# Kernel tuning notes

Hardware: AMD Instinct MI355X
Metric: run time of the kernel (lower is better)

## Reference

```python
import jax, jax.numpy as jnp
import numpy as np

N_HEADS = 16
LN_EPS = 1e-5


def _rope(x, sin, cos):
    # Faithful to source: uses x.shape[0] (batch here) as 'length'.
    L = x.shape[0]
    x1, x2 = x[..., ::2], x[..., 1::2]
    c = cos[:L, None, :]  # broadcasts over dim 1 (seq)
    s = sin[:L, None, :]
    return jnp.concatenate([x1 * c - x2 * s, x1 * s + x2 * c], axis=-1)


def _layer_norm(x):
    m = jnp.mean(x, axis=-1, keepdims=True)
    v = jnp.var(x, axis=-1, keepdims=True)
    return (x - m) * jax.lax.rsqrt(v + LN_EPS)


def setup_inputs() -> dict:
    key = jax.random.key(0)
    ks = jax.random.split(key, 8)
    B, S, D = 2, 2048, 2048
    CTX = 2048
    x = jax.random.normal(ks[0], (B, S, D), dtype=jnp.float32)
    scale = 0.02
    Wq = jax.random.normal(ks[1], (D, D), dtype=jnp.float32) * scale
    Wk = jax.random.normal(ks[2], (D, D), dtype=jnp.float32) * scale
    Wv = jax.random.normal(ks[3], (D, D), dtype=jnp.float32) * scale
    W1 = jax.random.normal(ks[4], (D, 4 * D), dtype=jnp.float32) * scale
    b1 = jnp.zeros((4 * D,), dtype=jnp.float32)
    W2 = jax.random.normal(ks[5], (4 * D, D), dtype=jnp.float32) * scale
    b2 = jnp.zeros((D,), dtype=jnp.float32)
    inv_freq = 1.0 / (10000.0 ** (jnp.arange(0, D, 2, dtype=jnp.float32) / D))
    sinusoid = jnp.einsum('i,j->ij', jnp.arange(CTX, dtype=jnp.float32), inv_freq)
    sin = jnp.sin(sinusoid)
    cos = jnp.cos(sinusoid)
    return {"x": x, "Wq": Wq, "Wk": Wk, "Wv": Wv, "W1": W1, "b1": b1,
            "W2": W2, "b2": b2, "sin": sin, "cos": cos, "i": 0}


def reference(x, Wq, Wk, Wv, W1, b1, W2, b2, sin, cos, i):
    B, S, D = x.shape
    H = N_HEADS
    hd = D // H
    q = _rope(x @ Wq, sin, cos)
    k = _rope(x @ Wk, sin, cos)
    v = x @ Wv
    # [B,S,D] -> [B,H,S,hd]
    q = q.reshape(B, S, H, hd).transpose(0, 2, 1, 3)
    k = k.reshape(B, S, H, hd).transpose(0, 2, 1, 3)
    v = v.reshape(B, S, H, hd).transpose(0, 2, 1, 3)
    attn = jnp.einsum('bhqd,bhkd->bhqk', q, k) / jnp.sqrt(jnp.float32(hd))
    causal = jnp.tril(jnp.ones((S, S), dtype=bool))
    attn = jnp.where(causal[None, None], attn, -jnp.inf)
    attn = jax.nn.softmax(attn, axis=-1)
    out = jnp.einsum('bhqk,bhkd->bhqd', attn, v)
    out = out.transpose(0, 2, 1, 3).reshape(B, S, D)
    out = _layer_norm(out + x)
    h = jax.nn.gelu(out @ W1 + b1, approximate=False)
    out2 = _layer_norm(h @ W2 + b2 + out)
    return out2
```

## Files before the change

### kernel.cpp

```cpp
#include <hip/hip_runtime.h>
#include <hip/hip_bf16.h>
#include <math.h>
#include <stdint.h>

using bf16 = __hip_bfloat16;
typedef __attribute__((ext_vector_type(4))) float f32x4;
typedef __attribute__((ext_vector_type(8))) short s16x8;

#define MFMA16(a, b, c) __builtin_amdgcn_mfma_f32_16x16x32_bf16(a, b, c, 0, 0, 0)

__device__ __forceinline__ void gload_lds16(const void* g, void* l) {
    __builtin_amdgcn_global_load_lds(
        (const __attribute__((address_space(1))) void*)g,
        (__attribute__((address_space(3))) void*)l, 16, 0, 0);
}

struct alignas(16) bf16x8s { bf16 v[8]; };

__global__ void cvt_f32_bf16(const float* __restrict__ in, bf16* __restrict__ out, long n) {
    long i = ((long)blockIdx.x * 256 + threadIdx.x) * 8;
    if (i >= n) return;
    float4 a = *(const float4*)(in + i);
    float4 b = *(const float4*)(in + i + 4);
    bf16x8s r;
    r.v[0] = __float2bfloat16(a.x); r.v[1] = __float2bfloat16(a.y);
    r.v[2] = __float2bfloat16(a.z); r.v[3] = __float2bfloat16(a.w);
    r.v[4] = __float2bfloat16(b.x); r.v[5] = __float2bfloat16(b.y);
    r.v[6] = __float2bfloat16(b.z); r.v[7] = __float2bfloat16(b.w);
    *(bf16x8s*)(out + i) = r;
}

__global__ void transpose_cvt(const float* __restrict__ W, bf16* __restrict__ Wt, int K, int N) {
    __shared__ bf16 t[32][33];
    int tx = threadIdx.x & 31, ty = threadIdx.x >> 5;
    int n0 = blockIdx.x * 32, k0 = blockIdx.y * 32;
    #pragma unroll
    for (int r = ty; r < 32; r += 8)
        t[r][tx] = __float2bfloat16(W[(size_t)(k0 + r) * N + n0 + tx]);
    __syncthreads();
    #pragma unroll
    for (int r = ty; r < 32; r += 8)
        Wt[(size_t)(n0 + r) * K + k0 + tx] = t[tx][r];
}

template <int EPI, int SPLITK>
__global__ __launch_bounds__(256) void gemm_bt(
    const bf16* __restrict__ A, const bf16* __restrict__ Bt,
    void* __restrict__ C, const float* __restrict__ bias,
    const float* __restrict__ resid, int M, int N, int K)
{
    __shared__ __align__(16) bf16 As[128 * 32];
    __shared__ __align__(16) bf16 Bs[128 * 32];
    const int tid = threadIdx.x;
    const int wid = tid >> 6, lane = tid & 63;
    const int quad = lane >> 4, l16 = lane & 15;
    const int bm = blockIdx.x * 128, bn = blockIdx.y * 128;
    const int wm = (wid >> 1) * 64, wn = (wid & 1) * 64;
    const int KH = K / SPLITK;
    const int kbeg = blockIdx.z * KH, kend = kbeg + KH;

    f32x4 acc[4][4] = {};

    for (int k0 = kbeg; k0 < kend; k0 += 32) {
        __syncthreads();
        #pragma unroll
        for (int c = 0; c < 2; ++c) {
            int choff = (wid * 2 + c) << 10;
            int off = choff + lane * 16;
            int row = off >> 6;
            int col = (off & 63) >> 1;
            gload_lds16(A  + (size_t)(bm + row) * K + k0 + col, (char*)As + choff);
            gload_lds16(Bt + (size_t)(bn + row) * K + k0 + col, (char*)Bs + choff);
        }
        __syncthreads();
        s16x8 af[4], bfr[4];
        #pragma unroll
        for (int mt = 0; mt < 4; ++mt)
            af[mt] = *(const s16x8*)(As + (wm + mt * 16 + l16) * 32 + quad * 8);
        #pragma unroll
        for (int nt = 0; nt < 4; ++nt)
            bfr[nt] = *(const s16x8*)(Bs + (wn + nt * 16 + l16) * 32 + quad * 8);
        #pragma unroll
        for (int mt = 0; mt < 4; ++mt)
            #pragma unroll
            for (int nt = 0; nt < 4; ++nt)
                acc[mt][nt] = MFMA16(af[mt], bfr[nt], acc[mt][nt]);
    }

    float* Cp = (float*)C;
    if (EPI == 3) Cp += (size_t)blockIdx.z * M * N;

    #pragma unroll
    for (int mt = 0; mt < 4; ++mt) {
        #pragma unroll
        for (int nt = 0; nt < 4; ++nt) {
            #pragma unroll
            for (int r = 0; r < 4; ++r) {
                int row = bm + wm + mt * 16 + quad * 4 + r;
                int col = bn + wn + nt * 16 + l16;
                float v = acc[mt][nt][r];
                if (EPI == 0) {
                    ((bf16*)C)[(size_t)row * N + col] = __float2bfloat16(v);
                } else if (EPI == 1) {
                    float xx = v + bias[col];
                    float g = 0.5f * xx * (1.0f + erff(xx * 0.7071067811865475f));
                    ((bf16*)C)[(size_t)row * N + col] = __float2bfloat16(g);
                } else if (EPI == 2) {
                    ((float*)C)[(size_t)row * N + col] =
                        v + bias[col] + resid[(size_t)row * N + col];
                } else {
                    Cp[(size_t)row * N + col] = v;
                }
            }
        }
    }
}

__global__ void rope_kernel(const bf16* __restrict__ in, bf16* __restrict__ out,
                            const float* __restrict__ sn, const float* __restrict__ cs,
                            int S, int D, int instride) {
    int row = blockIdx.x;
    int pos = row / S;
    const int half = D >> 1;
    const bf16* r = in + (size_t)row * instride;
    bf16* o = out + (size_t)row * D;
    for (int j = threadIdx.x; j < half; j += 256) {
        uint32_t pr = *(const uint32_t*)(r + 2 * j);
        float x1 = __uint_as_float(pr << 16);
        float x2 = __uint_as_float(pr & 0xffff0000u);
        float c = cs[(size_t)pos * half + j], s = sn[(size_t)pos * half + j];
        o[j]        = __float2bfloat16(x1 * c - x2 * s);
        o[half + j] = __float2bfloat16(x1 * s + x2 * c);
    }
}

__global__ void vtrans_kernel(const bf16* __restrict__ v, bf16* __restrict__ vt,
                              int S, int D, int H, int instride) {
    __shared__ bf16 t[32][33];
    int bh = blockIdx.z, b = bh >> 4, h = bh & 15;
    int s0 = blockIdx.x * 32, d0 = blockIdx.y * 32;
    int tx = threadIdx.x & 31, ty = threadIdx.x >> 5;
    #pragma unroll
    for (int r = ty; r < 32; r += 8)
        t[r][tx] = v[(size_t)(b * S + s0 + r) * instride + h * 128 + d0 + tx];
    __syncthreads();
    #pragma unroll
    for (int r = ty; r < 32; r += 8)
        vt[((size_t)bh * 128 + d0 + r) * S + s0 + tx] = t[tx][r];
}

__global__ __launch_bounds__(256, 4) void attn_kernel(
    const bf16* __restrict__ q, const bf16* __restrict__ k, const bf16* __restrict__ vt,
    float* __restrict__ o, int S, int D, int H)
{
    __shared__ __align__(16) char smem[40960];
    bf16* Ks = (bf16*)smem;
    bf16* Vs = (bf16*)(smem + 16384);
    bf16* Ps = (bf16*)(smem + 32768);

    const int tid = threadIdx.x, wid = tid >> 6, lane = tid & 63;
    const int quad = lane >> 4, l16 = lane & 15;
    const int bh = blockIdx.x, b = bh >> 4, h = bh & 15;
    const int qt = gridDim.y - 1 - blockIdx.y;
    const float scale = 0.08838834764831845f;

    s16x8 qf[4];
    const bf16* qrow = q + ((size_t)(b * S + qt * 64 + wid * 16 + l16)) * D + h * 128;
    #pragma unroll
    for (int ks = 0; ks < 4; ++ks)
        qf[ks] = *(const s16x8*)(qrow + ks * 32 + quad * 8);

    f32x4 oacc[8] = {};
    float mstate = -INFINITY, lstate = 0.f;

    const bf16* kb0 = k + (size_t)(b * S) * D + h * 128;
    const bf16* vb0 = vt + (size_t)bh * 128 * S;
    bf16* psw = Ps + wid * 16 * 64;
    const int sw = l16 & 7;
    const int nch = qt + 1;

    for (int kc = 0; kc < nch; ++kc) {
        __syncthreads();
        #pragma unroll
        for (int c = 0; c < 4; ++c) {
            int choff = (wid * 4 + c) << 10;
            int off = choff + lane * 16;
            int rk = off >> 8, bk = (off & 255) >> 4;
            gload_lds16(kb0 + (size_t)(kc * 64 + rk) * D + ((bk ^ (rk & 7)) << 3),
                        (char*)Ks + choff);
            int rv = off >> 7, bv = (off & 127) >> 4;
            gload_lds16(vb0 + (size_t)rv * S + kc * 64 + ((bv ^ (rv & 7)) << 3),
                        (char*)Vs + choff);
        }
        __syncthreads();

        f32x4 sacc[4] = {};
        #pragma unroll
        for (int mt = 0; mt < 4; ++mt) {
            #pragma unroll
            for (int ks = 0; ks < 4; ++ks) {
                s16x8 kf = *(const s16x8*)(Ks + (mt * 16 + l16) * 128 +
                                           (((ks * 4 + quad) ^ sw) << 3));
                sacc[mt] = MFMA16(kf, qf[ks], sacc[mt]);
            }
        }

        const bool need_mask = (kc == qt);
        #pragma unroll
        for (int mt = 0; mt < 4; ++mt)
            #pragma unroll
            for (int r = 0; r < 4; ++r) {
                float vv = sacc[mt][r] * scale;
                if (need_mask) {
                    int kl = mt * 16 + quad * 4 + r;
                    if (kl > wid * 16 + l16) vv = -INFINITY;
                }
                sacc[mt][r] = vv;
            }

        float mx = fmaxf(fmaxf(fmaxf(sacc[0][0], sacc[0][1]), fmaxf(sacc[0][2], sacc[0][3])),
                         fmaxf(fmaxf(sacc[1][0], sacc[1][1]), fmaxf(sacc[1][2], sacc[1][3])));
        mx = fmaxf(mx, fmaxf(fmaxf(fmaxf(sacc[2][0], sacc[2][1]), fmaxf(sacc[2][2], sacc[2][3])),
                             fmaxf(fmaxf(sacc[3][0], sacc[3][1]), fmaxf(sacc[3][2], sacc[3][3]))));
        mx = fmaxf(mx, __shfl_xor(mx, 16, 64));
        mx = fmaxf(mx, __shfl_xor(mx, 32, 64));
        float mnew = fmaxf(mstate, mx);
        float alpha = __expf(mstate - mnew);
        float rs = 0.f;
        #pragma unroll
        for (int mt = 0; mt < 4; ++mt)
            #pragma unroll
            for (int r = 0; r < 4; ++r) {
                float p = __expf(sacc[mt][r] - mnew);
                sacc[mt][r] = p;
                rs += p;
            }
        rs += __shfl_xor(rs, 16, 64);
        rs += __shfl_xor(rs, 32, 64);
        lstate = lstate * alpha + rs;
        mstate = mnew;
        #pragma unroll
        for (int mt = 0; mt < 8; ++mt)
            #pragma unroll
            for (int r = 0; r < 4; ++r) oacc[mt][r] *= alpha;

        #pragma unroll
        for (int mt = 0; mt < 4; ++mt)
            #pragma unroll
            for (int r = 0; r < 4; ++r) {
                int kl = mt * 16 + quad * 4 + r;
                psw[l16 * 64 + (((kl >> 3) ^ sw) << 3) + (kl & 7)] =
                    __float2bfloat16(sacc[mt][r]);
            }

        #pragma unroll
        for (int ks2 = 0; ks2 < 2; ++ks2) {
            s16x8 pf = *(const s16x8*)(psw + l16 * 64 + (((ks2 * 4 + quad) ^ sw) << 3));
            #pragma unroll
            for (int mt = 0; mt < 8; ++mt) {
                s16x8 vf = *(const s16x8*)(Vs + (mt * 16 + l16) * 64 +
                                           (((ks2 * 4 + quad) ^ sw) << 3));
                oacc[mt] = MFMA16(vf, pf, oacc[mt]);
            }
        }
    }

    float inv = 1.0f / lstate;
    __syncthreads();
    float* osw = (float*)smem + wid * 16 * 130;
    #pragma unroll
    for (int mt = 0; mt < 8; ++mt)
        #pragma unroll
        for (int r = 0; r < 4; ++r)
            osw[l16 * 130 + mt * 16 + quad * 4 + r] = oacc[mt][r] * inv;
    float* obase = o + (size_t)(b * S + qt * 64 + wid * 16) * D + h * 128;
    #pragma unroll
    for (int r16 = 0; r16 < 16; ++r16) {
        float2 val = *(const float2*)(osw + r16 * 130 + lane * 2);
        *(float2*)(obase + (size_t)r16 * D + lane * 2) = val;
    }
}

__global__ __launch_bounds__(256) void ln_kernel(
    const float* __restrict__ a, const float* __restrict__ b,
    const float* __restrict__ c, const float* __restrict__ bias,
    float* __restrict__ outf, bf16* __restrict__ outb, int D)
{
    int row = blockIdx.x;
    const float* pa = a + (size_t)row * D;
    const float* pb = b ? b + (size_t)row * D : nullptr;
    const float* pc = c ? c + (size_t)row * D : nullptr;
    float v[8];
    float sum = 0.f, sq = 0.f;
    #pragma unroll
    for (int u = 0; u < 8; ++u) {
        int j = threadIdx.x + u * 256;
        float x = pa[j];
        if (pb) x += pb[j];
        if (pc) x += pc[j];
        if (bias) x += bias[j];
        v[u] = x; sum += x; sq += x * x;
    }
    #pragma unroll
    for (int off = 32; off > 0; off >>= 1) {
        sum += __shfl_down(sum, off, 64);
        sq  += __shfl_down(sq,  off, 64);
    }
    __shared__ float red[8];
    int wid = threadIdx.x >> 6, lane = threadIdx.x & 63;
    if (lane == 0) { red[wid] = sum; red[4 + wid] = sq; }
    __syncthreads();
    sum = red[0] + red[1] + red[2] + red[3];
    sq  = red[4] + red[5] + red[6] + red[7];
    float mean = sum / D;
    float var = sq / D - mean * mean;
    float rstd = rsqrtf(fmaxf(var, 0.f) + 1e-5f);
    float* pof = outf ? outf + (size_t)row * D : nullptr;
    bf16* pob = outb ? outb + (size_t)row * D : nullptr;
    #pragma unroll
    for (int u = 0; u < 8; ++u) {
        int j = threadIdx.x + u * 256;
        float y = (v[u] - mean) * rstd;
        if (pof) pof[j] = y;
        if (pob) pob[j] = __float2bfloat16(y);
    }
}

extern "C" void kernel_launch(void* const* d_in, const int* in_sizes, int n_in,
                              void* d_out, int out_size, void* d_ws, size_t ws_size,
                              hipStream_t stream) {
    const float* x  = (const float*)d_in[0];
    const float* Wq = (const float*)d_in[1];
    const float* Wk = (const float*)d_in[2];
    const float* Wv = (const float*)d_in[3];
    const float* W1 = (const float*)d_in[4];
    const float* b1 = (const float*)d_in[5];
    const float* W2 = (const float*)d_in[6];
    const float* b2 = (const float*)d_in[7];
    const float* sn = (const float*)d_in[8];
    const float* cs = (const float*)d_in[9];

    const int B = 2, S = 2048, D = 2048, H = 16, Dff = 8192;
    const int M = B * S;
    const int NQKV = 3 * D;
    char* ws = (char*)d_ws;
    const size_t MB = 1024 * 1024;

    const size_t o_xb   = 0;
    const size_t o_Wqkv = 16 * MB;
    const size_t o_qkv  = 40 * MB;
    const size_t o_qr   = 0;
    const size_t o_kr   = 16 * MB;
    const size_t o_vt   = 88 * MB;
    const size_t o_attn = 40 * MB;
    const size_t o_outb = 0;
    const size_t o_outf = 72 * MB;
    const size_t o_W1t  = 16 * MB;
    const size_t o_h    = 104 * MB;
    const size_t o_W2t  = 16 * MB;
    const size_t o_p    = 168 * MB;

    long nx = (long)M * D;
    cvt_f32_bf16<<<nx / 2048, 256, 0, stream>>>(x, (bf16*)(ws + o_xb), nx);
    transpose_cvt<<<dim3(D / 32, D / 32), 256, 0, stream>>>(
        Wq, (bf16*)(ws + o_Wqkv), D, D);
    transpose_cvt<<<dim3(D / 32, D / 32), 256, 0, stream>>>(
        Wk, (bf16*)(ws + o_Wqkv) + (size_t)D * D, D, D);
    transpose_cvt<<<dim3(D / 32, D / 32), 256, 0, stream>>>(
        Wv, (bf16*)(ws + o_Wqkv) + 2 * (size_t)D * D, D, D);

    gemm_bt<0, 1><<<dim3(M / 128, NQKV / 128), 256, 0, stream>>>(
        (bf16*)(ws + o_xb), (bf16*)(ws + o_Wqkv), ws + o_qkv, nullptr, nullptr,
        M, NQKV, D);

    rope_kernel<<<M, 256, 0, stream>>>((bf16*)(ws + o_qkv), (bf16*)(ws + o_qr),
                                       sn, cs, S, D, NQKV);
    rope_kernel<<<M, 256, 0, stream>>>((bf16*)(ws + o_qkv) + D, (bf16*)(ws + o_kr),
                                       sn, cs, S, D, NQKV);
    vtrans_kernel<<<dim3(S / 32, 4, B * H), 256, 0, stream>>>(
        (bf16*)(ws + o_qkv) + 2 * D, (bf16*)(ws + o_vt), S, D, H, NQKV);

    attn_kernel<<<dim3(B * H, S / 64), 256, 0, stream>>>(
        (bf16*)(ws + o_qr), (bf16*)(ws + o_kr), (bf16*)(ws + o_vt),
        (float*)(ws + o_attn), S, D, H);

    ln_kernel<<<M, 256, 0, stream>>>((float*)(ws + o_attn), x, nullptr, nullptr,
                                     (float*)(ws + o_outf), (bf16*)(ws + o_outb), D);

    transpose_cvt<<<dim3(Dff / 32, D / 32), 256, 0, stream>>>(
        W1, (bf16*)(ws + o_W1t), D, Dff);
    gemm_bt<1, 1><<<dim3(M / 128, Dff / 128), 256, 0, stream>>>(
        (bf16*)(ws + o_outb), (bf16*)(ws + o_W1t), ws + o_h, b1, nullptr, M, Dff, D);

    transpose_cvt<<<dim3(D / 32, Dff / 32), 256, 0, stream>>>(
        W2, (bf16*)(ws + o_W2t), Dff, D);
    gemm_bt<3, 2><<<dim3(M / 128, D / 128, 2), 256, 0, stream>>>(
        (bf16*)(ws + o_h), (bf16*)(ws + o_W2t), ws + o_p, nullptr, nullptr, M, D, Dff);

    ln_kernel<<<M, 256, 0, stream>>>((float*)(ws + o_p),
                                     (float*)(ws + o_p) + (size_t)M * D,
                                     (float*)(ws + o_outf), b2,
                                     (float*)d_out, nullptr, D);
}
```

Measured before the change: 945.4 us.

## Replace GEMM with triple-buffered, XOR-swizzled 256x128 tile pipeline

Replaces the single-buffered 128x128 bf16 GEMM with a 512-thread kernel using 256x128 tiles, K-step 64, and a three-stage LDS ring fed by async global-to-LDS loads issued two tiles ahead. It adds an XOR swizzle on LDS columns to avoid bank conflicts, a remap of workgroup indices across the eight XCDs, and s_setprio around the MFMA bursts. The aim is to hide global-load latency and cut LDS stalls in the QKV, FFN1 and FFN2 GEMMs. The cost is 144KB of LDS per block, which limits occupancy to one block per CU, plus hand-written vmcnt waits that must match the number of loads in flight.

```diff
diff --git a/kernel.cpp b/kernel.cpp
--- a/kernel.cpp
+++ b/kernel.cpp
@@ -43,49 +43,112 @@
         Wt[(size_t)(n0 + r) * K + k0 + tx] = t[tx][r];
 }
 
+#define GEMM_LDS (3 * 49152)
+
 template <int EPI, int SPLITK>
-__global__ __launch_bounds__(256) void gemm_bt(
+__global__ __launch_bounds__(512) void gemm_pipe(
     const bf16* __restrict__ A, const bf16* __restrict__ Bt,
     void* __restrict__ C, const float* __restrict__ bias,
     const float* __restrict__ resid, int M, int N, int K)
 {
-    __shared__ __align__(16) bf16 As[128 * 32];
-    __shared__ __align__(16) bf16 Bs[128 * 32];
+    __shared__ __align__(16) char smem[GEMM_LDS];
     const int tid = threadIdx.x;
     const int wid = tid >> 6, lane = tid & 63;
     const int quad = lane >> 4, l16 = lane & 15;
-    const int bm = blockIdx.x * 128, bn = blockIdx.y * 128;
-    const int wm = (wid >> 1) * 64, wn = (wid & 1) * 64;
+
+    const int nx = gridDim.x;
+    const int nwg = nx * gridDim.y;
+    int lin = blockIdx.y * nx + blockIdx.x;
+    const int cpx = nwg >> 3;
+    lin = (lin & 7) * cpx + (lin >> 3);
+    const int bm = (lin % nx) * 256, bn = (lin / nx) * 128;
+
+    const int wrow = (wid >> 1) * 64;
+    const int wcol = (wid & 1) * 64;
     const int KH = K / SPLITK;
-    const int kbeg = blockIdx.z * KH, kend = kbeg + KH;
+    const int kbeg = blockIdx.z * KH;
+    const int NT = KH / 64;
+
+    const int soff = tid * 16;
+    const int ar0 = soff >> 7;
+    const int agc = ((((soff >> 4) & 7) ^ (ar0 & 7)) << 3);
+    const bf16* Ab = A + (size_t)(bm + ar0) * K + kbeg + agc;
+    const bf16* Bb = Bt + (size_t)(bn + ar0) * K + kbeg + agc;
+
+    const int asw = l16 & 7;
+    const int ko0 = (quad ^ asw) << 3;
+    const int ko1 = ((4 + quad) ^ asw) << 3;
+    const int arb = (wrow + l16) * 64;
+    const int brb = (wcol + l16) * 64;
 
     f32x4 acc[4][4] = {};
 
-    for (int k0 = kbeg; k0 < kend; k0 += 32) {
-        __syncthreads();
-        #pragma unroll
-        for (int c = 0; c < 2; ++c) {
-            int choff = (wid * 2 + c) << 10;
-            int off = choff + lane * 16;
-            int row = off >> 6;
-            int col = (off & 63) >> 1;
-            gload_lds16(A  + (size_t)(bm + row) * K + k0 + col, (char*)As + choff);
-            gload_lds16(Bt + (size_t)(bn + row) * K + k0 + col, (char*)Bs + choff);
-        }
-        __syncthreads();
-        s16x8 af[4], bfr[4];
-        #pragma unroll
-        for (int mt = 0; mt < 4; ++mt)
-            af[mt] = *(const s16x8*)(As + (wm + mt * 16 + l16) * 32 + quad * 8);
+#define STAGE_A(tt, dst) { \
+    _Pragma("unroll") \
+    for (int c = 0; c < 4; ++c) \
+        gload_lds16(Ab + (size_t)(c * 64) * K + (tt) * 64, \
+                    (dst) + wid * 1024 + c * 8192); }
+#define STAGE_B(tt, dst) { \
+    _Pragma("unroll") \
+    for (int c = 0; c < 2; ++c) \
+        gload_lds16(Bb + (size_t)(c * 64) * K + (tt) * 64, \
+                    (dst) + wid * 1024 + c * 8192); }
+
+    STAGE_A(0, smem);
+    STAGE_B(0, smem + 32768);
+    STAGE_A(1, smem + 49152);
+    STAGE_B(1, smem + 49152 + 32768);
+    asm volatile("s_waitcnt vmcnt(6)\ns_barrier" ::: "memory");
+
+    int st = 0;
+    for (int t = 0; t < NT; ++t) {
+        char* base = smem + st * 49152;
+        const bf16* As = (const bf16*)base;
+        const bf16* Bs = (const bf16*)(base + 32768);
+        int s2 = st + 2; if (s2 >= 3) s2 -= 3;
+        char* pre = smem + s2 * 49152;
+        const bool doPre = (t + 2 < NT);
+
+        s16x8 a0[4], b0[4];
+        #pragma unroll
+        for (int mt = 0; mt < 4; ++mt)
+            a0[mt] = *(const s16x8*)(As + arb + mt * 1024 + ko0);
         #pragma unroll
         for (int nt = 0; nt < 4; ++nt)
-            bfr[nt] = *(const s16x8*)(Bs + (wn + nt * 16 + l16) * 32 + quad * 8);
+            b0[nt] = *(const s16x8*)(Bs + brb + nt * 1024 + ko0);
+        if (doPre) STAGE_A(t + 2, pre);
+        __builtin_amdgcn_s_barrier();
+        __builtin_amdgcn_s_setprio(1);
         #pragma unroll
         for (int mt = 0; mt < 4; ++mt)
             #pragma unroll
             for (int nt = 0; nt < 4; ++nt)
-                acc[mt][nt] = MFMA16(af[mt], bfr[nt], acc[mt][nt]);
-    }
+                acc[mt][nt] = MFMA16(a0[mt], b0[nt], acc[mt][nt]);
+        __builtin_amdgcn_s_setprio(0);
+        __builtin_amdgcn_s_barrier();
+
+        s16x8 a1[4], b1[4];
+        #pragma unroll
+        for (int mt = 0; mt < 4; ++mt)
+            a1[mt] = *(const s16x8*)(As + arb + mt * 1024 + ko1);
+        #pragma unroll
+        for (int nt = 0; nt < 4; ++nt)
+            b1[nt] = *(const s16x8*)(Bs + brb + nt * 1024 + ko1);
+        if (doPre) STAGE_B(t + 2, pre + 32768);
+        __builtin_amdgcn_s_barrier();
+        __builtin_amdgcn_s_setprio(1);
+        #pragma unroll
+        for (int mt = 0; mt < 4; ++mt)
+            #pragma unroll
+            for (int nt = 0; nt < 4; ++nt)
+                acc[mt][nt] = MFMA16(a1[mt], b1[nt], acc[mt][nt]);
+        __builtin_amdgcn_s_setprio(0);
+        if (doPre) { asm volatile("s_waitcnt vmcnt(6)\ns_barrier" ::: "memory"); }
+        else       { asm volatile("s_waitcnt vmcnt(0)\ns_barrier" ::: "memory"); }
+        st = st + 1 == 3 ? 0 : st + 1;
+    }
+#undef STAGE_A
+#undef STAGE_B
 
     float* Cp = (float*)C;
     if (EPI == 3) Cp += (size_t)blockIdx.z * M * N;
@@ -96,8 +159,8 @@
         for (int nt = 0; nt < 4; ++nt) {
             #pragma unroll
             for (int r = 0; r < 4; ++r) {
-                int row = bm + wm + mt * 16 + quad * 4 + r;
-                int col = bn + wn + nt * 16 + l16;
+                int row = bm + wrow + mt * 16 + quad * 4 + r;
+                int col = bn + wcol + nt * 16 + l16;
                 float v = acc[mt][nt][r];
                 if (EPI == 0) {
                     ((bf16*)C)[(size_t)row * N + col] = __float2bfloat16(v);
@@ -369,7 +432,7 @@
     transpose_cvt<<<dim3(D / 32, D / 32), 256, 0, stream>>>(
         Wv, (bf16*)(ws + o_Wqkv) + 2 * (size_t)D * D, D, D);
 
-    gemm_bt<0, 1><<<dim3(M / 128, NQKV / 128), 256, 0, stream>>>(
+    gemm_pipe<0, 1><<<dim3(M / 256, NQKV / 128), 512, 0, stream>>>(
         (bf16*)(ws + o_xb), (bf16*)(ws + o_Wqkv), ws + o_qkv, nullptr, nullptr,
         M, NQKV, D);
 
@@ -389,12 +452,12 @@
 
     transpose_cvt<<<dim3(Dff / 32, D / 32), 256, 0, stream>>>(
         W1, (bf16*)(ws + o_W1t), D, Dff);
-    gemm_bt<1, 1><<<dim3(M / 128, Dff / 128), 256, 0, stream>>>(
+    gemm_pipe<1, 1><<<dim3(M / 256, Dff / 128), 512, 0, stream>>>(
         (bf16*)(ws + o_outb), (bf16*)(ws + o_W1t), ws + o_h, b1, nullptr, M, Dff, D);
 
     transpose_cvt<<<dim3(D / 32, Dff / 32), 256, 0, stream>>>(
         W2, (bf16*)(ws + o_W2t), Dff, D);
-    gemm_bt<3, 2><<<dim3(M / 128, D / 128, 2), 256, 0, stream>>>(
+    gemm_pipe<3, 2><<<dim3(M / 256, D / 128, 2), 512, 0, stream>>>(
         (bf16*)(ws + o_h), (bf16*)(ws + o_W2t), ws + o_p, nullptr, nullptr, M, D, Dff);
 
     ln_kernel<<<M, 256, 0, stream>>>((float*)(ws + o_p),
```

Result: faster. 833.9 us (-11.8%).

## Replace GEMM with 256x256 double-buffered pipelined kernel using swizzled LDS

Applied to the files above, without the earlier changes.

Replaces the simple 128x128 single-buffered GEMM with a 512-thread, 256x256-tile kernel that double-buffers 64-wide K slices in 128KB of LDS. Global-to-LDS loads for the next slice are interleaved with MFMA work on the current slice, using explicit vmcnt waits, barriers and setprio. It also XOR-swizzles the LDS layout to avoid bank conflicts and remaps block IDs across XCDs for cache locality. The aim is to hide memory latency and raise MFMA utilisation. The cost is larger tiles and heavy LDS use, which cut occupancy and leave fewer blocks for the split-K W2 GEMM.

```diff
diff --git a/kernel.cpp b/kernel.cpp
--- a/kernel.cpp
+++ b/kernel.cpp
@@ -43,62 +43,141 @@
         Wt[(size_t)(n0 + r) * K + k0 + tx] = t[tx][r];
 }
 
+#define GEMM_LDS 131072
+
 template <int EPI, int SPLITK>
-__global__ __launch_bounds__(256) void gemm_bt(
+__global__ __launch_bounds__(512) void gemm_pipe(
     const bf16* __restrict__ A, const bf16* __restrict__ Bt,
     void* __restrict__ C, const float* __restrict__ bias,
     const float* __restrict__ resid, int M, int N, int K)
 {
-    __shared__ __align__(16) bf16 As[128 * 32];
-    __shared__ __align__(16) bf16 Bs[128 * 32];
+    __shared__ __align__(16) char smem[GEMM_LDS];
     const int tid = threadIdx.x;
     const int wid = tid >> 6, lane = tid & 63;
     const int quad = lane >> 4, l16 = lane & 15;
-    const int bm = blockIdx.x * 128, bn = blockIdx.y * 128;
-    const int wm = (wid >> 1) * 64, wn = (wid & 1) * 64;
+    const int wm = wid >> 2, wn = wid & 3;
+
+    const int nx = gridDim.x;
+    const int nwg = nx * gridDim.y;
+    int lin = blockIdx.y * nx + blockIdx.x;
+    const int cpx = nwg >> 3;
+    lin = (lin & 7) * cpx + (lin >> 3);
+    const int bm = (lin % nx) * 256, bn = (lin / nx) * 256;
+
     const int KH = K / SPLITK;
-    const int kbeg = blockIdx.z * KH, kend = kbeg + KH;
-
-    f32x4 acc[4][4] = {};
-
-    for (int k0 = kbeg; k0 < kend; k0 += 32) {
-        __syncthreads();
-        #pragma unroll
-        for (int c = 0; c < 2; ++c) {
-            int choff = (wid * 2 + c) << 10;
-            int off = choff + lane * 16;
-            int row = off >> 6;
-            int col = (off & 63) >> 1;
-            gload_lds16(A  + (size_t)(bm + row) * K + k0 + col, (char*)As + choff);
-            gload_lds16(Bt + (size_t)(bn + row) * K + k0 + col, (char*)Bs + choff);
+    const int kbeg = blockIdx.z * KH;
+    const int NT = KH / 64;
+
+    const int r0 = tid >> 3, pb = tid & 7;
+    const int gcol = ((pb ^ (r0 & 7)) << 3);
+    const bf16* pA[2][2];
+    const bf16* pB[2][2];
+    #pragma unroll
+    for (int h = 0; h < 2; ++h)
+        #pragma unroll
+        for (int j = 0; j < 2; ++j) {
+            pA[h][j] = A + (size_t)(bm + h * 64 + j * 128 + r0) * K + kbeg + gcol;
+            pB[h][j] = Bt + (size_t)(bn + ((r0 >> 5) + 2 * j) * 64 + h * 32 + (r0 & 31)) * K
+                       + kbeg + gcol;
         }
-        __syncthreads();
-        s16x8 af[4], bfr[4];
-        #pragma unroll
-        for (int mt = 0; mt < 4; ++mt)
-            af[mt] = *(const s16x8*)(As + (wm + mt * 16 + l16) * 32 + quad * 8);
-        #pragma unroll
-        for (int nt = 0; nt < 4; ++nt)
-            bfr[nt] = *(const s16x8*)(Bs + (wn + nt * 16 + l16) * 32 + quad * 8);
-        #pragma unroll
-        for (int mt = 0; mt < 4; ++mt)
-            #pragma unroll
-            for (int nt = 0; nt < 4; ++nt)
-                acc[mt][nt] = MFMA16(af[mt], bfr[nt], acc[mt][nt]);
-    }
+    const int dA0 = tid * 16;
+    const int dA1 = 16384 + tid * 16;
+    const int dB0 = 32768 + tid * 16;
+    const int dB1 = 49152 + tid * 16;
+
+#define ST_A(h, base, T1) { \
+    gload_lds16(pA[h][0] + (T1) * 64, smem + (base)); \
+    gload_lds16(pA[h][1] + (T1) * 64, smem + (base) + 8192); }
+#define ST_B(h, base, T1) { \
+    gload_lds16(pB[h][0] + (T1) * 64, smem + (base)); \
+    gload_lds16(pB[h][1] + (T1) * 64, smem + (base) + 8192); }
+
+    const int asw = l16 & 7;
+    const int kx0 = (quad ^ asw) << 3;
+    const int kx1 = ((4 + quad) ^ asw) << 3;
+    const int aq0 = wm * 4096 + l16 * 64;
+    const int aq1 = (2 + wm) * 4096 + l16 * 64;
+    const int bq0 = 16384 + wn * 2048 + l16 * 64;
+    const int bq1 = bq0 + 8192;
+
+#define LDA(base) { _Pragma("unroll") for (int mt = 0; mt < 4; ++mt) { \
+    aF[0][mt] = *(const s16x8*)(sa + (base) + mt * 1024 + kx0); \
+    aF[1][mt] = *(const s16x8*)(sa + (base) + mt * 1024 + kx1); } }
+#define LDB(base) { _Pragma("unroll") for (int nt = 0; nt < 2; ++nt) { \
+    bF[0][nt] = *(const s16x8*)(sa + (base) + nt * 1024 + kx0); \
+    bF[1][nt] = *(const s16x8*)(sa + (base) + nt * 1024 + kx1); } }
+#define MM(mo, no) { \
+    __builtin_amdgcn_s_setprio(1); \
+    _Pragma("unroll") for (int kh = 0; kh < 2; ++kh) \
+    _Pragma("unroll") for (int mt = 0; mt < 4; ++mt) \
+    _Pragma("unroll") for (int nt = 0; nt < 2; ++nt) \
+        acc[(mo) + mt][(no) + nt] = MFMA16(aF[kh][mt], bF[kh][nt], acc[(mo) + mt][(no) + nt]); \
+    __builtin_amdgcn_s_setprio(0); }
+
+    f32x4 acc[8][4] = {};
+    s16x8 aF[2][4], bF[2][2];
+
+    ST_A(0, dA0, 0); ST_B(0, dB0, 0);
+    ST_A(1, dA1, 0);
+    ST_B(1, dB1, 0);
+    asm volatile("s_waitcnt vmcnt(4)" ::: "memory");
+    __builtin_amdgcn_s_barrier();
+
+    for (int t = 0; t < NT - 1; ++t) {
+        const int sl = t & 1;
+        const bf16* sa = (const bf16*)smem + sl * 32768;
+        const int sb1 = (sl ^ 1) * 65536;
+        LDA(aq0); LDB(bq0);
+        ST_A(0, sb1 + dA0, t + 1); ST_B(0, sb1 + dB0, t + 1);
+        MM(0, 0);
+        asm volatile("s_waitcnt vmcnt(6)" ::: "memory");
+        __builtin_amdgcn_s_barrier();
+        LDA(aq1);
+        ST_A(1, sb1 + dA1, t + 1);
+        MM(4, 0);
+        asm volatile("s_waitcnt vmcnt(6)" ::: "memory");
+        __builtin_amdgcn_s_barrier();
+        LDB(bq1);
+        ST_B(1, sb1 + dB1, t + 1);
+        MM(4, 2);
+        LDA(aq0);
+        MM(0, 2);
+        asm volatile("s_waitcnt vmcnt(4)" ::: "memory");
+        __builtin_amdgcn_s_barrier();
+    }
+    {
+        const bf16* sa = (const bf16*)smem + ((NT - 1) & 1) * 32768;
+        LDA(aq0); LDB(bq0);
+        MM(0, 0);
+        asm volatile("s_waitcnt vmcnt(2)" ::: "memory");
+        __builtin_amdgcn_s_barrier();
+        LDA(aq1);
+        MM(4, 0);
+        asm volatile("s_waitcnt vmcnt(0)" ::: "memory");
+        __builtin_amdgcn_s_barrier();
+        LDB(bq1);
+        MM(4, 2);
+        LDA(aq0);
+        MM(0, 2);
+    }
+#undef ST_A
+#undef ST_B
+#undef LDA
+#undef LDB
+#undef MM
 
     float* Cp = (float*)C;
     if (EPI == 3) Cp += (size_t)blockIdx.z * M * N;
 
     #pragma unroll
-    for (int mt = 0; mt < 4; ++mt) {
-        #pragma unroll
-        for (int nt = 0; nt < 4; ++nt) {
+    for (int m = 0; m < 8; ++m) {
+        #pragma unroll
+        for (int n = 0; n < 4; ++n) {
             #pragma unroll
             for (int r = 0; r < 4; ++r) {
-                int row = bm + wm + mt * 16 + quad * 4 + r;
-                int col = bn + wn + nt * 16 + l16;
-                float v = acc[mt][nt][r];
+                int row = bm + wm * 128 + m * 16 + quad * 4 + r;
+                int col = bn + wn * 64 + n * 16 + l16;
+                float v = acc[m][n][r];
                 if (EPI == 0) {
                     ((bf16*)C)[(size_t)row * N + col] = __float2bfloat16(v);
                 } else if (EPI == 1) {
@@ -369,7 +448,7 @@
     transpose_cvt<<<dim3(D / 32, D / 32), 256, 0, stream>>>(
         Wv, (bf16*)(ws + o_Wqkv) + 2 * (size_t)D * D, D, D);
 
-    gemm_bt<0, 1><<<dim3(M / 128, NQKV / 128), 256, 0, stream>>>(
+    gemm_pipe<0, 1><<<dim3(M / 256, NQKV / 256), 512, 0, stream>>>(
         (bf16*)(ws + o_xb), (bf16*)(ws + o_Wqkv), ws + o_qkv, nullptr, nullptr,
         M, NQKV, D);
 
@@ -389,12 +468,12 @@
 
     transpose_cvt<<<dim3(Dff / 32, D / 32), 256, 0, stream>>>(
         W1, (bf16*)(ws + o_W1t), D, Dff);
-    gemm_bt<1, 1><<<dim3(M / 128, Dff / 128), 256, 0, stream>>>(
+    gemm_pipe<1, 1><<<dim3(M / 256, Dff / 256), 512, 0, stream>>>(
         (bf16*)(ws + o_outb), (bf16*)(ws + o_W1t), ws + o_h, b1, nullptr, M, Dff, D);
 
     transpose_cvt<<<dim3(D / 32, Dff / 32), 256, 0, stream>>>(
         W2, (bf16*)(ws + o_W2t), Dff, D);
-    gemm_bt<3, 2><<<dim3(M / 128, D / 128, 2), 256, 0, stream>>>(
+    gemm_pipe<3, 2><<<dim3(M / 256, D / 256, 2), 512, 0, stream>>>(
         (bf16*)(ws + o_h), (bf16*)(ws + o_W2t), ws + o_p, nullptr, nullptr, M, D, Dff);
 
     ln_kernel<<<M, 256, 0, stream>>>((float*)(ws + o_p),
```

New measurement: 781.5 us. 1.21x faster.
